# Kernel tuning notes

Hardware: AMD Instinct MI355X
Metric: run time of the kernel (lower is better)

Reference implementation:

```python
import jax, jax.numpy as jnp
import numpy as np

B, S, SIZE = 2048, 512, 96  # size = embedding_size(32) * num_feature(3)


def setup_inputs() -> dict:
    key = jax.random.key(0)
    k1, k2, k3, k4, k5, k6, k7 = jax.random.split(key, 7)
    bound = 1.0 / np.sqrt(SIZE)  # nn.Linear default init range
    return {
        "seq_item_embedding": jax.random.normal(k1, (B, S, SIZE), dtype=jnp.float32),
        "target_item_embedding": jax.random.normal(k2, (B, 1, SIZE), dtype=jnp.float32),
        "mask": jax.random.randint(k3, (B, S + 1, 1), 0, 2).astype(jnp.bool_),
        "w1_weight": jax.random.uniform(k4, (SIZE, SIZE), jnp.float32, -bound, bound),
        "w1_bias": jax.random.uniform(k5, (SIZE,), jnp.float32, -bound, bound),
        "w2_weight": jax.random.uniform(k6, (SIZE, SIZE), jnp.float32, -bound, bound),
        "w2_bias": jax.random.uniform(k7, (SIZE,), jnp.float32, -bound, bound),
    }


def reference(seq_item_embedding, target_item_embedding, mask,
              w1_weight, w1_bias, w2_weight, w2_bias):
    # mask[:, :-1, :] -> [B, S] boolean (True = masked out)
    m = mask[:, :-1, 0]
    # w1(seq): [B, S, size]; note source reassigns seq_item_embedding to this,
    # so the final weighted pool uses the projected sequence.
    seq_h = jnp.einsum('bsd,ed->bse', seq_item_embedding, w1_weight) + w1_bias
    # w2(target): [B, 1, size], broadcasts over seq_len (repeat in torch)
    tgt_h = jnp.einsum('bqd,ed->bqe', target_item_embedding, w2_weight) + w2_bias
    # sigmoid(sum) reduced over feature dim -> scores [B, S]
    scores = jax.nn.sigmoid(seq_h + tgt_h).sum(axis=-1)
    scores = jnp.where(m, jnp.float32(-1e9), scores)
    attn = jax.nn.softmax(scores, axis=-1)  # [B, S]
    # weighted pool over seq dim -> [B, size]
    output = jnp.einsum('bs,bse->be', attn, seq_h)
    return output
```

## Files before the change

kernel.cpp:

```cpp
#include <hip/hip_runtime.h>
#include <math.h>

#define NB 2048
#define NS 512
#define ND 96

typedef __attribute__((ext_vector_type(8))) short short8;
typedef __attribute__((ext_vector_type(4))) float floatx4;

__device__ __forceinline__ unsigned f2bfu(float f) {
    union { float f; unsigned u; } c; c.f = f;
    unsigned u = c.u;
    u += 0x7FFF + ((u >> 16) & 1);
    return u >> 16;
}
__device__ __forceinline__ unsigned pack2(float a, float b) {
    return f2bfu(a) | (f2bfu(b) << 16);
}
__device__ __forceinline__ float lo_f(unsigned u) {
    union { unsigned u; float f; } c; c.u = u << 16; return c.f;
}
__device__ __forceinline__ float hi_f(unsigned u) {
    union { unsigned u; float f; } c; c.u = u & 0xFFFF0000u; return c.f;
}
__device__ __forceinline__ float sigm(float x) {
    return 1.0f / (1.0f + __expf(-x));
}

__global__ __launch_bounds__(512, 4)
void attn_fused(const float* __restrict__ seq,
                const float* __restrict__ tgt,
                const int*   __restrict__ mask,
                const float* __restrict__ w1,
                const float* __restrict__ b1,
                const float* __restrict__ w2,
                const float* __restrict__ b2,
                float* __restrict__ out)
{
    __shared__ short w1f[18 * 64 * 8];
    __shared__ float sc[NS];
    __shared__ float at[NS];
    __shared__ float th[ND];
    __shared__ float red1[8], red2[8];
    __shared__ float osum[8][ND];

    const int b    = blockIdx.x;
    const int tid  = threadIdx.x;
    const int lane = tid & 63;
    const int wave = tid >> 6;
    const int l15  = lane & 15;
    const int quad = lane >> 4;

    for (int idx = tid; idx < 1152; idx += 512) {
        const int e  = idx / 12;
        const int dc = idx - 12 * e;
        const int kk = dc >> 2;
        const int q  = dc & 3;
        const float* p = w1 + e * ND + kk * 32 + q * 8;
        floatx4 p0 = *(const floatx4*)(p);
        floatx4 p1 = *(const floatx4*)(p + 4);
        short8 v;
        v[0]=(short)f2bfu(p0[0]); v[1]=(short)f2bfu(p0[1]);
        v[2]=(short)f2bfu(p0[2]); v[3]=(short)f2bfu(p0[3]);
        v[4]=(short)f2bfu(p1[0]); v[5]=(short)f2bfu(p1[1]);
        v[6]=(short)f2bfu(p1[2]); v[7]=(short)f2bfu(p1[3]);
        const int t = e >> 4, r = e & 15;
        *(short8*)&w1f[(((t * 3 + kk) * 64) + q * 16 + r) * 8] = v;
    }

    if (tid < ND) {
        const float* tv = tgt + (size_t)b * ND;
        const float* wr = w2 + tid * ND;
        float acc = b2[tid];
        #pragma unroll
        for (int d = 0; d < ND; d += 4) {
            acc += tv[d]*wr[d] + tv[d+1]*wr[d+1] + tv[d+2]*wr[d+2] + tv[d+3]*wr[d+3];
        }
        th[tid] = acc;
    }
    __syncthreads();

    float tgtv[6], biasv[6];
    #pragma unroll
    for (int t = 0; t < 6; ++t) {
        tgtv[t]  = th[16 * t + l15];
        biasv[t] = b1[16 * t + l15];
    }

    unsigned pk[4][6][2];
    const float* abase = seq + ((size_t)b * NS + l15) * ND + quad * 8;

    #pragma unroll
    for (int sti = 0; sti < 4; ++sti) {
        const int s0 = (wave * 4 + sti) * 16;
        short8 af[3];
        #pragma unroll
        for (int kk = 0; kk < 3; ++kk) {
            const float* p = abase + (size_t)s0 * ND + kk * 32;
            floatx4 p0 = *(const floatx4*)(p);
            floatx4 p1 = *(const floatx4*)(p + 4);
            short8 v;
            v[0]=(short)f2bfu(p0[0]); v[1]=(short)f2bfu(p0[1]);
            v[2]=(short)f2bfu(p0[2]); v[3]=(short)f2bfu(p0[3]);
            v[4]=(short)f2bfu(p1[0]); v[5]=(short)f2bfu(p1[1]);
            v[6]=(short)f2bfu(p1[2]); v[7]=(short)f2bfu(p1[3]);
            af[kk] = v;
        }
        float p0s = 0.f, p1s = 0.f, p2s = 0.f, p3s = 0.f;
        #pragma unroll
        for (int t = 0; t < 6; ++t) {
            floatx4 acc = { biasv[t], biasv[t], biasv[t], biasv[t] };
            #pragma unroll
            for (int kk = 0; kk < 3; ++kk) {
                const short8 bf = *(const short8*)&w1f[((t * 3 + kk) * 64 + lane) * 8];
                acc = __builtin_amdgcn_mfma_f32_16x16x32_bf16(af[kk], bf, acc, 0, 0, 0);
            }
            pk[sti][t][0] = pack2(acc[0], acc[1]);
            pk[sti][t][1] = pack2(acc[2], acc[3]);
            const float thv = tgtv[t];
            p0s += sigm(acc[0] + thv);
            p1s += sigm(acc[1] + thv);
            p2s += sigm(acc[2] + thv);
            p3s += sigm(acc[3] + thv);
        }
        #pragma unroll
        for (int off = 1; off < 16; off <<= 1) {
            p0s += __shfl_xor(p0s, off, 64);
            p1s += __shfl_xor(p1s, off, 64);
            p2s += __shfl_xor(p2s, off, 64);
            p3s += __shfl_xor(p3s, off, 64);
        }
        if (l15 == 0) {
            sc[s0 + quad * 4 + 0] = p0s;
            sc[s0 + quad * 4 + 1] = p1s;
            sc[s0 + quad * 4 + 2] = p2s;
            sc[s0 + quad * 4 + 3] = p3s;
        }
    }
    __syncthreads();

    float v = sc[tid];
    if (mask[(size_t)b * (NS + 1) + tid] != 0) v = -1e9f;
    float mx = v;
    #pragma unroll
    for (int off = 1; off < 64; off <<= 1) mx = fmaxf(mx, __shfl_xor(mx, off, 64));
    if (lane == 0) red1[wave] = mx;
    __syncthreads();
    mx = red1[0];
    #pragma unroll
    for (int w = 1; w < 8; ++w) mx = fmaxf(mx, red1[w]);
    const float e0 = __expf(v - mx);
    float ssum = e0;
    #pragma unroll
    for (int off = 1; off < 64; off <<= 1) ssum += __shfl_xor(ssum, off, 64);
    if (lane == 0) red2[wave] = ssum;
    __syncthreads();
    float tot = red2[0];
    #pragma unroll
    for (int w = 1; w < 8; ++w) tot += red2[w];
    at[tid] = e0 * (1.0f / tot);
    __syncthreads();

    float o[6] = {0.f, 0.f, 0.f, 0.f, 0.f, 0.f};
    #pragma unroll
    for (int sti = 0; sti < 4; ++sti) {
        const int s0 = (wave * 4 + sti) * 16 + quad * 4;
        const float a0 = at[s0], a1 = at[s0 + 1], a2 = at[s0 + 2], a3 = at[s0 + 3];
        #pragma unroll
        for (int t = 0; t < 6; ++t) {
            const unsigned u0 = pk[sti][t][0];
            const unsigned u1 = pk[sti][t][1];
            o[t] += a0 * lo_f(u0) + a1 * hi_f(u0) + a2 * lo_f(u1) + a3 * hi_f(u1);
        }
    }
    #pragma unroll
    for (int t = 0; t < 6; ++t) {
        o[t] += __shfl_xor(o[t], 16, 64);
        o[t] += __shfl_xor(o[t], 32, 64);
    }
    if (quad == 0) {
        #pragma unroll
        for (int t = 0; t < 6; ++t) osum[wave][16 * t + l15] = o[t];
    }
    __syncthreads();
    if (tid < ND) {
        float a = 0.f;
        #pragma unroll
        for (int w = 0; w < 8; ++w) a += osum[w][tid];
        out[(size_t)b * ND + tid] = a;
    }
}

extern "C" void kernel_launch(void* const* d_in, const int* in_sizes, int n_in,
                              void* d_out, int out_size, void* d_ws, size_t ws_size,
                              hipStream_t stream) {
    const float* seq  = (const float*)d_in[0];
    const float* tgt  = (const float*)d_in[1];
    const int*   mask = (const int*)d_in[2];
    const float* w1   = (const float*)d_in[3];
    const float* b1   = (const float*)d_in[4];
    const float* w2   = (const float*)d_in[5];
    const float* b2   = (const float*)d_in[6];
    float* out = (float*)d_out;
    attn_fused<<<dim3(NB), dim3(512), 0, stream>>>(seq, tgt, mask, w1, b1, w2, b2, out);
}
```

Baseline: 589.7 us.

## Stage sequence tiles through LDS and keep projected sequence in shared memory

Doubles the block to 1024 threads with each wave handling half the output features. Sequence rows are loaded coalesced in 128-row chunks, converted to bf16 into an LDS staging tile, and fed to MFMA from there. The projected sequence is written to a large bf16 LDS buffer instead of registers, and the final weighted pool is done by per-feature threads reading from LDS. This aims to improve global load coalescing and reduce register pressure. In exchange it uses far more shared memory, limiting blocks per CU, and adds per-chunk barriers.

Result: no change. 592.1 us (+0.4%).

```diff
diff --git a/kernel.cpp b/kernel.cpp
--- a/kernel.cpp
+++ b/kernel.cpp
@@ -4,9 +4,12 @@
 #define NB 2048
 #define NS 512
 #define ND 96
+#define ST_H 100
+#define ST_S 104
 
 typedef __attribute__((ext_vector_type(8))) short short8;
 typedef __attribute__((ext_vector_type(4))) float floatx4;
+typedef __attribute__((ext_vector_type(2))) unsigned uint2v;
 
 __device__ __forceinline__ unsigned f2bfu(float f) {
     union { float f; unsigned u; } c; c.f = f;
@@ -17,17 +20,16 @@
 __device__ __forceinline__ unsigned pack2(float a, float b) {
     return f2bfu(a) | (f2bfu(b) << 16);
 }
-__device__ __forceinline__ float lo_f(unsigned u) {
-    union { unsigned u; float f; } c; c.u = u << 16; return c.f;
-}
-__device__ __forceinline__ float hi_f(unsigned u) {
-    union { unsigned u; float f; } c; c.u = u & 0xFFFF0000u; return c.f;
+__device__ __forceinline__ float bf2f(short s) {
+    union { unsigned u; float f; } c;
+    c.u = ((unsigned)(unsigned short)s) << 16;
+    return c.f;
 }
 __device__ __forceinline__ float sigm(float x) {
     return 1.0f / (1.0f + __expf(-x));
 }
 
-__global__ __launch_bounds__(512, 4)
+__global__ __launch_bounds__(1024, 4)
 void attn_fused(const float* __restrict__ seq,
                 const float* __restrict__ tgt,
                 const int*   __restrict__ mask,
@@ -37,11 +39,13 @@
                 const float* __restrict__ b2,
                 float* __restrict__ out)
 {
+    __shared__ short sh[NS * ST_H];
+    __shared__ short stg[128 * ST_S];
     __shared__ short w1f[18 * 64 * 8];
-    __shared__ float sc[NS];
-    __shared__ float at[NS];
+    __shared__ float sc2[2][NS];
+    __shared__ float atn[NS];
     __shared__ float th[ND];
-    __shared__ float red1[8], red2[8];
+    __shared__ float red1[16], red2[16];
     __shared__ float osum[8][ND];
 
     const int b    = blockIdx.x;
@@ -50,8 +54,11 @@
     const int wave = tid >> 6;
     const int l15  = lane & 15;
     const int quad = lane >> 4;
-
-    for (int idx = tid; idx < 1152; idx += 512) {
+    const int tile  = wave & 7;
+    const int ehalf = wave >> 3;
+    const int tbase = ehalf * 3;
+
+    for (int idx = tid; idx < 1152; idx += 1024) {
         const int e  = idx / 12;
         const int dc = idx - 12 * e;
         const int kk = dc >> 2;
@@ -80,67 +87,78 @@
     }
     __syncthreads();
 
-    float tgtv[6], biasv[6];
-    #pragma unroll
-    for (int t = 0; t < 6; ++t) {
-        tgtv[t]  = th[16 * t + l15];
-        biasv[t] = b1[16 * t + l15];
-    }
-
-    unsigned pk[4][6][2];
-    const float* abase = seq + ((size_t)b * NS + l15) * ND + quad * 8;
-
-    #pragma unroll
-    for (int sti = 0; sti < 4; ++sti) {
-        const int s0 = (wave * 4 + sti) * 16;
+    float tgtv[3], biasv[3];
+    #pragma unroll
+    for (int j = 0; j < 3; ++j) {
+        tgtv[j]  = th[16 * (tbase + j) + l15];
+        biasv[j] = b1[16 * (tbase + j) + l15];
+    }
+
+    for (int c = 0; c < 4; ++c) {
+        const float* gbase = seq + ((size_t)b * NS + c * 128) * ND;
+        #pragma unroll
+        for (int i = 0; i < 3; ++i) {
+            const int fi = (tid + i * 1024) * 4;
+            floatx4 v = *(const floatx4*)(gbase + fi);
+            const int r   = fi / 96;
+            const int col = fi - 96 * r;
+            uint2v pkd;
+            pkd[0] = pack2(v[0], v[1]);
+            pkd[1] = pack2(v[2], v[3]);
+            *(uint2v*)&stg[r * ST_S + col] = pkd;
+        }
+        __syncthreads();
+
         short8 af[3];
         #pragma unroll
         for (int kk = 0; kk < 3; ++kk) {
-            const float* p = abase + (size_t)s0 * ND + kk * 32;
-            floatx4 p0 = *(const floatx4*)(p);
-            floatx4 p1 = *(const floatx4*)(p + 4);
-            short8 v;
-            v[0]=(short)f2bfu(p0[0]); v[1]=(short)f2bfu(p0[1]);
-            v[2]=(short)f2bfu(p0[2]); v[3]=(short)f2bfu(p0[3]);
-            v[4]=(short)f2bfu(p1[0]); v[5]=(short)f2bfu(p1[1]);
-            v[6]=(short)f2bfu(p1[2]); v[7]=(short)f2bfu(p1[3]);
-            af[kk] = v;
-        }
-        float p0s = 0.f, p1s = 0.f, p2s = 0.f, p3s = 0.f;
-        #pragma unroll
-        for (int t = 0; t < 6; ++t) {
-            floatx4 acc = { biasv[t], biasv[t], biasv[t], biasv[t] };
+            af[kk] = *(const short8*)&stg[(tile * 16 + l15) * ST_S + kk * 32 + quad * 8];
+        }
+
+        float ps0 = 0.f, ps1 = 0.f, ps2 = 0.f, ps3 = 0.f;
+        const int s0 = c * 128 + tile * 16;
+        #pragma unroll
+        for (int j = 0; j < 3; ++j) {
+            const int t = tbase + j;
+            floatx4 acc = { biasv[j], biasv[j], biasv[j], biasv[j] };
             #pragma unroll
             for (int kk = 0; kk < 3; ++kk) {
                 const short8 bf = *(const short8*)&w1f[((t * 3 + kk) * 64 + lane) * 8];
                 acc = __builtin_amdgcn_mfma_f32_16x16x32_bf16(af[kk], bf, acc, 0, 0, 0);
             }
-            pk[sti][t][0] = pack2(acc[0], acc[1]);
-            pk[sti][t][1] = pack2(acc[2], acc[3]);
-            const float thv = tgtv[t];
-            p0s += sigm(acc[0] + thv);
-            p1s += sigm(acc[1] + thv);
-            p2s += sigm(acc[2] + thv);
-            p3s += sigm(acc[3] + thv);
+            const int e = 16 * t + l15;
+            short* dst = &sh[(s0 + quad * 4) * ST_H + e];
+            dst[0]          = (short)f2bfu(acc[0]);
+            dst[ST_H]       = (short)f2bfu(acc[1]);
+            dst[2 * ST_H]   = (short)f2bfu(acc[2]);
+            dst[3 * ST_H]   = (short)f2bfu(acc[3]);
+            const float thv = tgtv[j];
+            ps0 += sigm(acc[0] + thv);
+            ps1 += sigm(acc[1] + thv);
+            ps2 += sigm(acc[2] + thv);
+            ps3 += sigm(acc[3] + thv);
         }
         #pragma unroll
         for (int off = 1; off < 16; off <<= 1) {
-            p0s += __shfl_xor(p0s, off, 64);
-            p1s += __shfl_xor(p1s, off, 64);
-            p2s += __shfl_xor(p2s, off, 64);
-            p3s += __shfl_xor(p3s, off, 64);
+            ps0 += __shfl_xor(ps0, off, 64);
+            ps1 += __shfl_xor(ps1, off, 64);
+            ps2 += __shfl_xor(ps2, off, 64);
+            ps3 += __shfl_xor(ps3, off, 64);
         }
         if (l15 == 0) {
-            sc[s0 + quad * 4 + 0] = p0s;
-            sc[s0 + quad * 4 + 1] = p1s;
-            sc[s0 + quad * 4 + 2] = p2s;
-            sc[s0 + quad * 4 + 3] = p3s;
-        }
-    }
-    __syncthreads();
-
-    float v = sc[tid];
-    if (mask[(size_t)b * (NS + 1) + tid] != 0) v = -1e9f;
+            sc2[ehalf][s0 + quad * 4 + 0] = ps0;
+            sc2[ehalf][s0 + quad * 4 + 1] = ps1;
+            sc2[ehalf][s0 + quad * 4 + 2] = ps2;
+            sc2[ehalf][s0 + quad * 4 + 3] = ps3;
+        }
+        __syncthreads();
+    }
+
+    float v = -1e30f;
+    if (tid < NS) {
+        v = sc2[0][tid] + sc2[1][tid];
+        if (mask[(size_t)b * (NS + 1) + tid] != 0) v = -1e9f;
+    }
     float mx = v;
     #pragma unroll
     for (int off = 1; off < 64; off <<= 1) mx = fmaxf(mx, __shfl_xor(mx, off, 64));
@@ -148,8 +166,8 @@
     __syncthreads();
     mx = red1[0];
     #pragma unroll
-    for (int w = 1; w < 8; ++w) mx = fmaxf(mx, red1[w]);
-    const float e0 = __expf(v - mx);
+    for (int w = 1; w < 16; ++w) mx = fmaxf(mx, red1[w]);
+    const float e0 = (tid < NS) ? __expf(v - mx) : 0.f;
     float ssum = e0;
     #pragma unroll
     for (int off = 1; off < 64; off <<= 1) ssum += __shfl_xor(ssum, off, 64);
@@ -157,36 +175,26 @@
     __syncthreads();
     float tot = red2[0];
     #pragma unroll
-    for (int w = 1; w < 8; ++w) tot += red2[w];
-    at[tid] = e0 * (1.0f / tot);
-    __syncthreads();
-
-    float o[6] = {0.f, 0.f, 0.f, 0.f, 0.f, 0.f};
-    #pragma unroll
-    for (int sti = 0; sti < 4; ++sti) {
-        const int s0 = (wave * 4 + sti) * 16 + quad * 4;
-        const float a0 = at[s0], a1 = at[s0 + 1], a2 = at[s0 + 2], a3 = at[s0 + 3];
-        #pragma unroll
-        for (int t = 0; t < 6; ++t) {
-            const unsigned u0 = pk[sti][t][0];
-            const unsigned u1 = pk[sti][t][1];
-            o[t] += a0 * lo_f(u0) + a1 * hi_f(u0) + a2 * lo_f(u1) + a3 * hi_f(u1);
-        }
-    }
-    #pragma unroll
-    for (int t = 0; t < 6; ++t) {
-        o[t] += __shfl_xor(o[t], 16, 64);
-        o[t] += __shfl_xor(o[t], 32, 64);
-    }
-    if (quad == 0) {
-        #pragma unroll
-        for (int t = 0; t < 6; ++t) osum[wave][16 * t + l15] = o[t];
+    for (int w = 1; w < 16; ++w) tot += red2[w];
+    if (tid < NS) atn[tid] = e0 * (1.0f / tot);
+    __syncthreads();
+
+    if (tid < 8 * ND) {
+        const int g = tid / ND;
+        const int e = tid - g * ND;
+        float acc = 0.f;
+        const int sb = g * 64;
+        #pragma unroll 4
+        for (int s = sb; s < sb + 64; ++s) {
+            acc += atn[s] * bf2f(sh[s * ST_H + e]);
+        }
+        osum[g][e] = acc;
     }
     __syncthreads();
     if (tid < ND) {
         float a = 0.f;
         #pragma unroll
-        for (int w = 0; w < 8; ++w) a += osum[w][tid];
+        for (int g = 0; g < 8; ++g) a += osum[g][tid];
         out[(size_t)b * ND + tid] = a;
     }
 }
@@ -202,5 +210,5 @@
     const float* w2   = (const float*)d_in[5];
     const float* b2   = (const float*)d_in[6];
     float* out = (float*)d_out;
-    attn_fused<<<dim3(NB), dim3(512), 0, stream>>>(seq, tgt, mask, w1, b1, w2, b2, out);
-}
+    attn_fused<<<dim3(NB), dim3(1024), 0, stream>>>(seq, tgt, mask, w1, b1, w2, b2, out);
+}
```
